# Kernel optimization log

Measured on AMD Instinct MI355X. Metric: run time of the kernel, lower is better.

The kernel has to match this reference:

```python
import jax, jax.numpy as jnp
import numpy as np

D_MODEL = 1024
D = 512
B = 32
L = 1024


def setup_inputs() -> dict:
    key = jax.random.key(0)
    ks = jax.random.split(key, 8)
    s = 1.0 / np.sqrt(D_MODEL)
    x = jax.random.normal(ks[0], (B, L, D_MODEL), dtype=jnp.float32)
    mask = jnp.ones((B, 1, L), dtype=jnp.int32)  # padding mask; 1 = keep
    Wq = jax.random.uniform(ks[1], (D, D_MODEL), jnp.float32, -s, s)
    bq = jax.random.uniform(ks[2], (D,), jnp.float32, -s, s)
    Wk = jax.random.uniform(ks[3], (D, D_MODEL), jnp.float32, -s, s)
    bk = jax.random.uniform(ks[4], (D,), jnp.float32, -s, s)
    Wv = jax.random.uniform(ks[5], (D, D_MODEL), jnp.float32, -s, s)
    bv = jax.random.uniform(ks[6], (D,), jnp.float32, -s, s)
    return {"x": x, "Wq": Wq, "bq": bq, "Wk": Wk, "bk": bk, "Wv": Wv, "bv": bv, "mask": mask}


def reference(x, Wq, bq, Wk, bk, Wv, bv, mask):
    Bq, Lq, _ = x.shape
    q = jnp.einsum('blc,dc->bld', x, Wq) + bq  # [B,L,D]
    k = jnp.einsum('blc,dc->bld', x, Wk) + bk
    v = jnp.einsum('blc,dc->bld', x, Wv) + bv
    scale = k.shape[-1] ** -0.5
    weights = jnp.einsum('bid,bjd->bij', q, k) * scale  # [B,L,L]
    causal = jnp.tril(jnp.ones((Lq, Lq), dtype=bool))
    neg_inf = jnp.float32(-jnp.inf)
    weights = jnp.where(causal[None, :, :], weights, neg_inf)
    weights = jnp.where(mask == 0, neg_inf, weights)  # mask broadcasts [B,1,L]
    weights = jax.nn.softmax(weights, axis=-1)
    # NOTE: source calls self.dropout(weights) but discards result -> no-op
    out = jnp.einsum('bij,bjd->bid', weights, v)
    return jax.nn.relu(out)
```

## Files before the change

### kernel.cpp

```cpp
#include <hip/hip_runtime.h>
#include <hip/hip_bf16.h>
#include <stdint.h>

#define DM 1024
#define DD 512
#define BB 32
#define LL 1024
#define SCALE 0.04419417382415922f
#define MAT ((size_t)BB * LL * DD)

typedef float f32x4 __attribute__((ext_vector_type(4)));
typedef short bf16x8 __attribute__((ext_vector_type(8)));
typedef short bf16x4 __attribute__((ext_vector_type(4)));

__device__ inline unsigned short f2bf(float f) {
    union { float f; uint32_t u; } v; v.f = f;
    uint32_t r = v.u + 0x7fffu + ((v.u >> 16) & 1u);
    return (unsigned short)(r >> 16);
}
__device__ inline float bf2f(unsigned short u) {
    union { uint32_t u; float f; } v; v.u = ((uint32_t)u) << 16;
    return v.f;
}

__device__ inline bf16x4 cvt4(f32x4 a, float s) {
    bf16x4 r;
    r[0] = (short)f2bf(a[0] * s);
    r[1] = (short)f2bf(a[1] * s);
    r[2] = (short)f2bf(a[2] * s);
    r[3] = (short)f2bf(a[3] * s);
    return r;
}

#define GLOAD_LDS16(gsrc, ldst) \
    __builtin_amdgcn_global_load_lds((const __attribute__((address_space(1))) unsigned int*)(gsrc), \
        (__attribute__((address_space(3))) unsigned int*)(ldst), 16, 0, 0)

__device__ inline void publish_barrier() {
    asm volatile("s_waitcnt vmcnt(0)" ::: "memory");
    __builtin_amdgcn_sched_barrier(0);
    __builtin_amdgcn_s_barrier();
    __builtin_amdgcn_sched_barrier(0);
}
__device__ inline void gate6() {
    asm volatile("s_waitcnt vmcnt(6)" ::: "memory");
    __builtin_amdgcn_sched_barrier(0);
    __builtin_amdgcn_s_barrier();
    __builtin_amdgcn_sched_barrier(0);
}
__device__ inline void gate4() {
    asm volatile("s_waitcnt vmcnt(4)" ::: "memory");
    __builtin_amdgcn_sched_barrier(0);
    __builtin_amdgcn_s_barrier();
    __builtin_amdgcn_sched_barrier(0);
}
__device__ inline void gate2() {
    asm volatile("s_waitcnt vmcnt(2)" ::: "memory");
    __builtin_amdgcn_sched_barrier(0);
    __builtin_amdgcn_s_barrier();
    __builtin_amdgcn_sched_barrier(0);
}
__device__ inline void gate0() {
    asm volatile("s_waitcnt vmcnt(0)" ::: "memory");
    __builtin_amdgcn_sched_barrier(0);
    __builtin_amdgcn_s_barrier();
    __builtin_amdgcn_sched_barrier(0);
}
__device__ inline void gateB() {
    __builtin_amdgcn_sched_barrier(0);
    __builtin_amdgcn_s_barrier();
    __builtin_amdgcn_sched_barrier(0);
}

__global__ __launch_bounds__(256) void cast_all(const float* __restrict__ x,
                                                const float* __restrict__ Wq,
                                                const float* __restrict__ Wk,
                                                const float* __restrict__ Wv,
                                                unsigned short* __restrict__ xb,
                                                unsigned short* __restrict__ Wb)
{
    int bx = blockIdx.x;
    if (bx < 16384) {
        size_t idx = (size_t)bx * 256 + threadIdx.x;
        size_t base = idx * 8;
        f32x4 a = *(const f32x4*)(x + base);
        f32x4 b = *(const f32x4*)(x + base + 4);
        bf16x4 lo = cvt4(a, 1.0f), hi = cvt4(b, 1.0f);
        bf16x8 o = {lo[0], lo[1], lo[2], lo[3], hi[0], hi[1], hi[2], hi[3]};
        *(bf16x8*)(xb + base) = o;
    } else {
        size_t idx = (size_t)(bx - 16384) * 256 + threadIdx.x;
        int o = (int)(idx >> 16);
        size_t rem = idx & 65535;
        const float* W = (o == 0) ? Wq : (o == 1) ? Wk : Wv;
        float s = (o == 0) ? SCALE : 1.0f;
        size_t base = rem * 8;
        f32x4 a = *(const f32x4*)(W + base);
        f32x4 b = *(const f32x4*)(W + base + 4);
        bf16x4 lo = cvt4(a, s), hi = cvt4(b, s);
        bf16x8 out = {lo[0], lo[1], lo[2], lo[3], hi[0], hi[1], hi[2], hi[3]};
        *(bf16x8*)(Wb + (size_t)o * 524288 + base) = out;
    }
}

__global__ __launch_bounds__(512, 2) void qkv_proj4(
    const unsigned short* __restrict__ xb,
    const unsigned short* __restrict__ Wb,
    const float* __restrict__ bq, const float* __restrict__ bk, const float* __restrict__ bv,
    unsigned short* __restrict__ qkv)
{
    __shared__ __align__(16) unsigned short AL[2][2][8192];
    __shared__ __align__(16) unsigned short BL[2][2][8192];

    const int o = blockIdx.y;
    const float* bias = (o == 0) ? bq : (o == 1) ? bk : bv;
    const float wscale = (o == 0) ? SCALE : 1.0f;
    const unsigned short* W = Wb + (size_t)o * 524288;
    unsigned short* out = qkv + (size_t)o * MAT;

    int wg = blockIdx.x;
    wg = (wg & 7) * 32 + (wg >> 3);
    const int mt = wg >> 1, nt = wg & 1;
    const int rowbase = mt * 256;
    const int colbase = nt * 256;

    const int tid  = threadIdx.x;
    const int lane = tid & 63;
    const int w    = tid >> 6;
    const int wm   = w >> 2;
    const int wn   = w & 3;
    const int l15  = lane & 15, l4 = lane >> 4;
    const int rxor = l15 & 7;

    const int r8   = lane >> 3;
    const int swch = (lane & 7) ^ r8;

    const char* xpanel = (const char*)(xb + (size_t)rowbase * DM);
    const char* wpanel = (const char*)(W  + (size_t)colbase * DM);

    #define STAGE_HALF(panel, T, H, slot) do {                                   \
        _Pragma("unroll")                                                        \
        for (int i2 = 0; i2 < 2; ++i2) {                                         \
            int grp = i2 * 8 + w;                                                \
            GLOAD_LDS16((panel) + ((size_t)((H) * 128 + grp * 8 + r8) * 2048)    \
                            + (size_t)(T) * 128 + swch * 16,                     \
                        (char*)(slot) + grp * 1024);                             \
        }                                                                        \
    } while (0)

    #define RDA(base, mf4, ks) (*(const bf16x8*)((base) + (wm * 64 + (mf4) * 16 + l15) * 128 \
                            + ((((ks) * 4 + l4) ^ rxor) << 4)))
    #define RDB(base, nfl, ks) (*(const bf16x8*)((base) + (wn * 32 + (nfl) * 16 + l15) * 128 \
                            + ((((ks) * 4 + l4) ^ rxor) << 4)))

    f32x4 acc[8][4];
    #pragma unroll
    for (int i = 0; i < 8; ++i)
        #pragma unroll
        for (int j = 0; j < 4; ++j)
            acc[i][j] = (f32x4){0.f, 0.f, 0.f, 0.f};

    bf16x8 aF[4][2], bF[4][2];

    STAGE_HALF(xpanel, 0, 0, &AL[0][0][0]);
    STAGE_HALF(wpanel, 0, 0, &BL[0][0][0]);
    STAGE_HALF(wpanel, 0, 1, &BL[0][1][0]);
    STAGE_HALF(xpanel, 0, 1, &AL[0][1][0]);

    for (int t = 0; t < 16; ++t) {
        const int c = t & 1, cn = c ^ 1;
        const char* A0b = (const char*)&AL[c][0][0];
        const char* A1b = (const char*)&AL[c][1][0];
        const char* B0b = (const char*)&BL[c][0][0];
        const char* B1b = (const char*)&BL[c][1][0];
        const bool st = (t < 15);

        if (st) { STAGE_HALF(xpanel, t + 1, 0, &AL[cn][0][0]); gate6(); } else gate4();
        #pragma unroll
        for (int ks = 0; ks < 2; ++ks) {
            #pragma unroll
            for (int mf = 0; mf < 4; ++mf) aF[mf][ks] = RDA(A0b, mf, ks);
            bF[0][ks] = RDB(B0b, 0, ks);
            bF[1][ks] = RDB(B0b, 1, ks);
        }
        __builtin_amdgcn_s_setprio(1);
        #pragma unroll
        for (int ks = 0; ks < 2; ++ks)
            #pragma unroll
            for (int nf = 0; nf < 2; ++nf)
                #pragma unroll
                for (int mf = 0; mf < 4; ++mf)
                    acc[mf][nf] = __builtin_amdgcn_mfma_f32_16x16x32_bf16(aF[mf][ks], bF[nf][ks], acc[mf][nf], 0, 0, 0);
        __builtin_amdgcn_s_setprio(0);

        if (st) { STAGE_HALF(wpanel, t + 1, 0, &BL[cn][0][0]); gate6(); } else gate2();
        #pragma unroll
        for (int ks = 0; ks < 2; ++ks) {
            bF[2][ks] = RDB(B1b, 0, ks);
            bF[3][ks] = RDB(B1b, 1, ks);
        }
        __builtin_amdgcn_s_setprio(1);
        #pragma unroll
        for (int ks = 0; ks < 2; ++ks)
            #pragma unroll
            for (int nf = 0; nf < 2; ++nf)
                #pragma unroll
                for (int mf = 0; mf < 4; ++mf)
                    acc[mf][2 + nf] = __builtin_amdgcn_mfma_f32_16x16x32_bf16(aF[mf][ks], bF[2 + nf][ks], acc[mf][2 + nf], 0, 0, 0);
        __builtin_amdgcn_s_setprio(0);

        if (st) { STAGE_HALF(wpanel, t + 1, 1, &BL[cn][1][0]); gate6(); } else gate0();
        #pragma unroll
        for (int ks = 0; ks < 2; ++ks)
            #pragma unroll
            for (int mf = 0; mf < 4; ++mf) aF[mf][ks] = RDA(A1b, mf, ks);
        __builtin_amdgcn_s_setprio(1);
        #pragma unroll
        for (int ks = 0; ks < 2; ++ks)
            #pragma unroll
            for (int nf = 0; nf < 2; ++nf)
                #pragma unroll
                for (int mf = 0; mf < 4; ++mf)
                    acc[4 + mf][nf] = __builtin_amdgcn_mfma_f32_16x16x32_bf16(aF[mf][ks], bF[nf][ks], acc[4 + mf][nf], 0, 0, 0);
        __builtin_amdgcn_s_setprio(0);

        if (st) STAGE_HALF(xpanel, t + 1, 1, &AL[cn][1][0]);
        gateB();
        __builtin_amdgcn_s_setprio(1);
        #pragma unroll
        for (int ks = 0; ks < 2; ++ks)
            #pragma unroll
            for (int nf = 0; nf < 2; ++nf)
                #pragma unroll
                for (int mf = 0; mf < 4; ++mf)
                    acc[4 + mf][2 + nf] = __builtin_amdgcn_mfma_f32_16x16x32_bf16(aF[mf][ks], bF[2 + nf][ks], acc[4 + mf][2 + nf], 0, 0, 0);
        __builtin_amdgcn_s_setprio(0);
    }
    #undef STAGE_HALF
    #undef RDA
    #undef RDB

    #pragma unroll
    for (int nf = 0; nf < 4; ++nf) {
        int col = colbase + ((nf < 2) ? wn * 32 + nf * 16 : 128 + wn * 32 + (nf - 2) * 16) + l15;
        float bv_ = bias[col] * wscale;
        #pragma unroll
        for (int mf = 0; mf < 8; ++mf) {
            int row0 = rowbase + ((mf < 4) ? wm * 64 + mf * 16 : 128 + wm * 64 + (mf - 4) * 16) + l4 * 4;
            #pragma unroll
            for (int r = 0; r < 4; ++r)
                out[(size_t)(row0 + r) * DD + col] = f2bf(acc[mf][nf][r] + bv_);
        }
    }
}

__global__ __launch_bounds__(256) void vtrans(const unsigned short* __restrict__ v,
                                              unsigned short* __restrict__ vt)
{
    __shared__ unsigned short T[64][72];
    const int lt = blockIdx.x, dt = blockIdx.y, b = blockIdx.z;
    const int t = threadIdx.x;
    const unsigned short* src = v + ((size_t)(b * LL + lt * 64)) * DD + dt * 64;
    #pragma unroll
    for (int it = 0; it < 2; ++it) {
        int r  = (t >> 3) + it * 32;
        int c0 = (t & 7) * 8;
        bf16x8 x = *(const bf16x8*)(src + (size_t)r * DD + c0);
        *(bf16x4*)&T[r][c0]     = (bf16x4){x[0], x[1], x[2], x[3]};
        *(bf16x4*)&T[r][c0 + 4] = (bf16x4){x[4], x[5], x[6], x[7]};
    }
    __syncthreads();
    unsigned short* dst = vt + ((size_t)(b * DD + dt * 64)) * LL + lt * 64;
    #pragma unroll
    for (int it = 0; it < 2; ++it) {
        int d  = (t >> 3) + it * 32;
        int c0 = (t & 7) * 8;
        bf16x8 o;
        #pragma unroll
        for (int e = 0; e < 8; ++e) o[e] = T[c0 + e][d];
        *(bf16x8*)(dst + (size_t)d * LL + c0) = o;
    }
}

__global__ __launch_bounds__(256, 2) void sgemm_qk(
    const unsigned short* __restrict__ qkv,
    unsigned short* __restrict__ S)
{
    __shared__ __align__(16) unsigned short At[2][8192];
    __shared__ __align__(16) unsigned short Bt[2][8192];

    int wg = blockIdx.x;
    wg = (wg & 7) * 144 + (wg >> 3);
    const int b = wg / 36;
    const int t36 = wg % 36;
    int mt = 0, accq = 0;
    while (accq + mt + 1 <= t36) { ++mt; accq += mt; }
    const int nt = t36 - accq;

    const int tid  = threadIdx.x;
    const int lane = tid & 63;
    const int w    = tid >> 6;
    const int wr   = (w >> 1) * 64;
    const int wc   = (w & 1) * 64;
    const int l15  = lane & 15, l4 = lane >> 4;

    const int r8   = lane >> 3;
    const int swch = (lane & 7) ^ r8;

    const unsigned short* q = qkv;
    const unsigned short* k = qkv + MAT;
    const char* apanel = (const char*)(q + ((size_t)(b * LL) + mt * 128) * DD);
    const char* bpanel = (const char*)(k + ((size_t)(b * LL) + nt * 128) * DD);

    f32x4 acc[4][4];
    #pragma unroll
    for (int i = 0; i < 4; ++i)
        #pragma unroll
        for (int j = 0; j < 4; ++j)
            acc[i][j] = (f32x4){0.f, 0.f, 0.f, 0.f};

    #define STAGE_QK(KK, BUF) do {                                               \
        _Pragma("unroll")                                                        \
        for (int i2 = 0; i2 < 4; ++i2) {                                         \
            int grp = i2 * 4 + w;                                                \
            size_t rowoff = (size_t)(grp * 8 + r8) * 1024 + (KK) * 2 + swch * 16;\
            GLOAD_LDS16(apanel + rowoff, (char*)&At[BUF][0] + grp * 1024);       \
            GLOAD_LDS16(bpanel + rowoff, (char*)&Bt[BUF][0] + grp * 1024);       \
        }                                                                        \
    } while (0)

    STAGE_QK(0, 0);
    __syncthreads();

    for (int t = 0; t < 8; ++t) {
        const int cur = t & 1;
        if (t < 7) STAGE_QK((t + 1) * 64, cur ^ 1);

        const char* Ab = (const char*)&At[cur][0];
        const char* Bb = (const char*)&Bt[cur][0];
        #pragma unroll
        for (int ks = 0; ks < 2; ++ks) {
            bf16x8 af[4], bf_[4];
            const int ch = (ks * 4 + l4) ^ (l15 & 7);
            #pragma unroll
            for (int m = 0; m < 4; ++m)
                af[m] = *(const bf16x8*)(Ab + (wr + m * 16 + l15) * 128 + (ch << 4));
            #pragma unroll
            for (int n = 0; n < 4; ++n)
                bf_[n] = *(const bf16x8*)(Bb + (wc + n * 16 + l15) * 128 + (ch << 4));
            #pragma unroll
            for (int n = 0; n < 4; ++n)
                #pragma unroll
                for (int m = 0; m < 4; ++m)
                    acc[m][n] = __builtin_amdgcn_mfma_f32_16x16x32_bf16(af[m], bf_[n], acc[m][n], 0, 0, 0);
        }

        if (t < 7) publish_barrier();
    }
    #undef STAGE_QK

    unsigned short* sp = S + ((size_t)(b * LL) + mt * 128) * LL + nt * 128;
    #pragma unroll
    for (int n = 0; n < 4; ++n) {
        int col = wc + n * 16 + l15;
        #pragma unroll
        for (int m = 0; m < 4; ++m) {
            int row0 = wr + m * 16 + l4 * 4;
            #pragma unroll
            for (int r = 0; r < 4; ++r)
                sp[(size_t)(row0 + r) * LL + col] = f2bf(acc[m][n][r]);
        }
    }
}

__global__ __launch_bounds__(256) void softmax_rows(
    const unsigned short* __restrict__ S,
    const int* __restrict__ mask,
    unsigned short* __restrict__ P)
{
    __shared__ float mbias[1024];
    const int rc = blockIdx.x, b = blockIdx.y;
    const int tid = threadIdx.x, lane = tid & 63, w = tid >> 6;

    {
        const int* mp = mask + b * LL;
        #pragma unroll
        for (int j = 0; j < 4; ++j)
            mbias[tid * 4 + j] = mp[tid * 4 + j] ? 0.0f : -1e30f;
    }
    __syncthreads();

    const int j0 = lane * 16;
    for (int i = 0; i < 32; ++i) {
        const int r = rc * 128 + i * 4 + w;
        const unsigned short* srow = S + ((size_t)(b * LL) + r) * LL;

        bf16x8 v0 = {0,0,0,0,0,0,0,0}, v1 = {0,0,0,0,0,0,0,0};
        if (j0 <= r)     v0 = *(const bf16x8*)(srow + j0);
        if (j0 + 8 <= r) v1 = *(const bf16x8*)(srow + j0 + 8);

        float s[16];
        #pragma unroll
        for (int e = 0; e < 8; ++e) {
            int j = j0 + e;
            s[e]     = (j <= r)     ? bf2f((unsigned short)v0[e]) + mbias[j]     : -3e38f;
            s[8 + e] = (j + 8 <= r) ? bf2f((unsigned short)v1[e]) + mbias[j + 8] : -3e38f;
        }
        float mx = s[0];
        #pragma unroll
        for (int e = 1; e < 16; ++e) mx = fmaxf(mx, s[e]);
        mx = fmaxf(mx, __shfl_xor(mx, 1));
        mx = fmaxf(mx, __shfl_xor(mx, 2));
        mx = fmaxf(mx, __shfl_xor(mx, 4));
        mx = fmaxf(mx, __shfl_xor(mx, 8));
        mx = fmaxf(mx, __shfl_xor(mx, 16));
        mx = fmaxf(mx, __shfl_xor(mx, 32));

        float p[16], ls = 0.f;
        #pragma unroll
        for (int e = 0; e < 16; ++e) { p[e] = __expf(s[e] - mx); ls += p[e]; }
        ls += __shfl_xor(ls, 1);
        ls += __shfl_xor(ls, 2);
        ls += __shfl_xor(ls, 4);
        ls += __shfl_xor(ls, 8);
        ls += __shfl_xor(ls, 16);
        ls += __shfl_xor(ls, 32);
        const float inv = 1.0f / ls;

        bf16x8 o0, o1;
        #pragma unroll
        for (int e = 0; e < 8; ++e) {
            o0[e] = (short)f2bf(p[e] * inv);
            o1[e] = (short)f2bf(p[8 + e] * inv);
        }
        unsigned short* prow = P + ((size_t)(b * LL) + r) * LL;
        *(bf16x8*)(prow + j0)     = o0;
        *(bf16x8*)(prow + j0 + 8) = o1;
    }
}

__global__ __launch_bounds__(256, 2) void pv_gemm(
    const unsigned short* __restrict__ P,
    const unsigned short* __restrict__ vt,
    float* __restrict__ outp)
{
    __shared__ __align__(16) unsigned short At[2][8192];
    __shared__ __align__(16) unsigned short Bt[2][8192];

    int wg = blockIdx.x;
    wg = (wg & 7) * 128 + (wg >> 3);
    const int b  = wg >> 5;
    const int rr = wg & 31;
    const int rt = 7 - (rr >> 2);
    const int ct = rr & 3;

    const int tid  = threadIdx.x;
    const int lane = tid & 63;
    const int w    = tid >> 6;
    const int wr   = (w >> 1) * 64;
    const int wc   = (w & 1) * 64;
    const int l15  = lane & 15, l4 = lane >> 4;

    const int r8   = lane >> 3;
    const int swch = (lane & 7) ^ r8;

    const char* apanel = (const char*)(P  + ((size_t)(b * LL) + rt * 128) * LL);
    const char* bpanel = (const char*)(vt + ((size_t)(b * DD) + ct * 128) * LL);

    const int NT = (rt + 1) * 2;

    f32x4 acc[4][4];
    #pragma unroll
    for (int i = 0; i < 4; ++i)
        #pragma unroll
        for (int j = 0; j < 4; ++j)
            acc[i][j] = (f32x4){0.f, 0.f, 0.f, 0.f};

    #define STAGE_PV(KK, BUF) do {                                               \
        _Pragma("unroll")                                                        \
        for (int i2 = 0; i2 < 4; ++i2) {                                         \
            int grp = i2 * 4 + w;                                                \
            size_t rowoff = (size_t)(grp * 8 + r8) * 2048 + (KK) * 2 + swch * 16;\
            GLOAD_LDS16(apanel + rowoff, (char*)&At[BUF][0] + grp * 1024);       \
            GLOAD_LDS16(bpanel + rowoff, (char*)&Bt[BUF][0] + grp * 1024);       \
        }                                                                        \
    } while (0)

    STAGE_PV(0, 0);
    __syncthreads();

    for (int t = 0; t < NT; ++t) {
        const int cur = t & 1;
        if (t < NT - 1) STAGE_PV((t + 1) * 64, cur ^ 1);

        const char* Ab = (const char*)&At[cur][0];
        const char* Bb = (const char*)&Bt[cur][0];
        #pragma unroll
        for (int ks = 0; ks < 2; ++ks) {
            bf16x8 af[4], bf_[4];
            const int ch = (ks * 4 + l4) ^ (l15 & 7);
            #pragma unroll
            for (int m = 0; m < 4; ++m)
                af[m] = *(const bf16x8*)(Ab + (wr + m * 16 + l15) * 128 + (ch << 4));
            #pragma unroll
            for (int n = 0; n < 4; ++n)
                bf_[n] = *(const bf16x8*)(Bb + (wc + n * 16 + l15) * 128 + (ch << 4));
            #pragma unroll
            for (int n = 0; n < 4; ++n)
                #pragma unroll
                for (int m = 0; m < 4; ++m)
                    acc[m][n] = __builtin_amdgcn_mfma_f32_16x16x32_bf16(af[m], bf_[n], acc[m][n], 0, 0, 0);
        }

        if (t < NT - 1) publish_barrier();
    }
    #undef STAGE_PV

    float* op = outp + ((size_t)(b * LL) + rt * 128) * DD + ct * 128;
    #pragma unroll
    for (int n = 0; n < 4; ++n) {
        int col = wc + n * 16 + l15;
        #pragma unroll
        for (int m = 0; m < 4; ++m) {
            int row0 = wr + m * 16 + l4 * 4;
            #pragma unroll
            for (int r = 0; r < 4; ++r)
                op[(size_t)(row0 + r) * DD + col] = fmaxf(acc[m][n][r], 0.f);
        }
    }
}

extern "C" void kernel_launch(void* const* d_in, const int* in_sizes, int n_in,
                              void* d_out, int out_size, void* d_ws, size_t ws_size,
                              hipStream_t stream) {
    const float* x  = (const float*)d_in[0];
    const float* Wq = (const float*)d_in[1];
    const float* bq = (const float*)d_in[2];
    const float* Wk = (const float*)d_in[3];
    const float* bk = (const float*)d_in[4];
    const float* Wv = (const float*)d_in[5];
    const float* bv = (const float*)d_in[6];
    const int* mask = (const int*)d_in[7];

    unsigned short* qkv = (unsigned short*)d_ws;
    unsigned short* v   = qkv + 2 * MAT;
    unsigned short* vtp = qkv + 3 * MAT;
    unsigned short* Wb  = vtp;
    unsigned short* xb  = (unsigned short*)d_out;
    unsigned short* S   = (unsigned short*)d_out;
    unsigned short* Pp  = qkv;
    float* out = (float*)d_out;

    cast_all<<<17152, 256, 0, stream>>>(x, Wq, Wk, Wv, xb, Wb);
    qkv_proj4<<<dim3(256, 3), 512, 0, stream>>>(xb, Wb, bq, bk, bv, qkv);
    vtrans<<<dim3(16, 8, 32), 256, 0, stream>>>(v, vtp);
    sgemm_qk<<<dim3(1152), 256, 0, stream>>>(qkv, S);
    softmax_rows<<<dim3(8, 32), 256, 0, stream>>>(S, mask, Pp);
    pv_gemm<<<dim3(1024), 256, 0, stream>>>(Pp, vtp, out);
}
```

Baseline: 282.0 us.

## Fuse V transpose into QKV projection epilogue and drop setprio hints

```diff
diff --git a/kernel.cpp b/kernel.cpp
--- a/kernel.cpp
+++ b/kernel.cpp
@@ -103,11 +103,12 @@
     }
 }
 
-__global__ __launch_bounds__(512, 2) void qkv_proj4(
+__global__ __launch_bounds__(512, 2) void qkv_proj5(
     const unsigned short* __restrict__ xb,
     const unsigned short* __restrict__ Wb,
     const float* __restrict__ bq, const float* __restrict__ bk, const float* __restrict__ bv,
-    unsigned short* __restrict__ qkv)
+    unsigned short* __restrict__ qkv,
+    unsigned short* __restrict__ vt)
 {
     __shared__ __align__(16) unsigned short AL[2][2][8192];
     __shared__ __align__(16) unsigned short BL[2][2][8192];
@@ -183,7 +184,6 @@
             bF[0][ks] = RDB(B0b, 0, ks);
             bF[1][ks] = RDB(B0b, 1, ks);
         }
-        __builtin_amdgcn_s_setprio(1);
         #pragma unroll
         for (int ks = 0; ks < 2; ++ks)
             #pragma unroll
@@ -191,7 +191,6 @@
                 #pragma unroll
                 for (int mf = 0; mf < 4; ++mf)
                     acc[mf][nf] = __builtin_amdgcn_mfma_f32_16x16x32_bf16(aF[mf][ks], bF[nf][ks], acc[mf][nf], 0, 0, 0);
-        __builtin_amdgcn_s_setprio(0);
 
         if (st) { STAGE_HALF(wpanel, t + 1, 0, &BL[cn][0][0]); gate6(); } else gate2();
         #pragma unroll
@@ -199,7 +198,6 @@
             bF[2][ks] = RDB(B1b, 0, ks);
             bF[3][ks] = RDB(B1b, 1, ks);
         }
-        __builtin_amdgcn_s_setprio(1);
         #pragma unroll
         for (int ks = 0; ks < 2; ++ks)
             #pragma unroll
@@ -207,14 +205,12 @@
                 #pragma unroll
                 for (int mf = 0; mf < 4; ++mf)
                     acc[mf][2 + nf] = __builtin_amdgcn_mfma_f32_16x16x32_bf16(aF[mf][ks], bF[2 + nf][ks], acc[mf][2 + nf], 0, 0, 0);
-        __builtin_amdgcn_s_setprio(0);
 
         if (st) { STAGE_HALF(wpanel, t + 1, 1, &BL[cn][1][0]); gate6(); } else gate0();
         #pragma unroll
         for (int ks = 0; ks < 2; ++ks)
             #pragma unroll
             for (int mf = 0; mf < 4; ++mf) aF[mf][ks] = RDA(A1b, mf, ks);
-        __builtin_amdgcn_s_setprio(1);
         #pragma unroll
         for (int ks = 0; ks < 2; ++ks)
             #pragma unroll
@@ -222,11 +218,9 @@
                 #pragma unroll
                 for (int mf = 0; mf < 4; ++mf)
                     acc[4 + mf][nf] = __builtin_amdgcn_mfma_f32_16x16x32_bf16(aF[mf][ks], bF[nf][ks], acc[4 + mf][nf], 0, 0, 0);
-        __builtin_amdgcn_s_setprio(0);
 
         if (st) STAGE_HALF(xpanel, t + 1, 1, &AL[cn][1][0]);
         gateB();
-        __builtin_amdgcn_s_setprio(1);
         #pragma unroll
         for (int ks = 0; ks < 2; ++ks)
             #pragma unroll
@@ -234,51 +228,63 @@
                 #pragma unroll
                 for (int mf = 0; mf < 4; ++mf)
                     acc[4 + mf][2 + nf] = __builtin_amdgcn_mfma_f32_16x16x32_bf16(aF[mf][ks], bF[2 + nf][ks], acc[4 + mf][2 + nf], 0, 0, 0);
-        __builtin_amdgcn_s_setprio(0);
     }
     #undef STAGE_HALF
     #undef RDA
     #undef RDB
 
-    #pragma unroll
-    for (int nf = 0; nf < 4; ++nf) {
-        int col = colbase + ((nf < 2) ? wn * 32 + nf * 16 : 128 + wn * 32 + (nf - 2) * 16) + l15;
-        float bv_ = bias[col] * wscale;
-        #pragma unroll
-        for (int mf = 0; mf < 8; ++mf) {
-            int row0 = rowbase + ((mf < 4) ? wm * 64 + mf * 16 : 128 + wm * 64 + (mf - 4) * 16) + l4 * 4;
-            #pragma unroll
-            for (int r = 0; r < 4; ++r)
-                out[(size_t)(row0 + r) * DD + col] = f2bf(acc[mf][nf][r] + bv_);
-        }
-    }
-}
-
-__global__ __launch_bounds__(256) void vtrans(const unsigned short* __restrict__ v,
-                                              unsigned short* __restrict__ vt)
-{
-    __shared__ unsigned short T[64][72];
-    const int lt = blockIdx.x, dt = blockIdx.y, b = blockIdx.z;
-    const int t = threadIdx.x;
-    const unsigned short* src = v + ((size_t)(b * LL + lt * 64)) * DD + dt * 64;
-    #pragma unroll
-    for (int it = 0; it < 2; ++it) {
-        int r  = (t >> 3) + it * 32;
-        int c0 = (t & 7) * 8;
-        bf16x8 x = *(const bf16x8*)(src + (size_t)r * DD + c0);
-        *(bf16x4*)&T[r][c0]     = (bf16x4){x[0], x[1], x[2], x[3]};
-        *(bf16x4*)&T[r][c0 + 4] = (bf16x4){x[4], x[5], x[6], x[7]};
-    }
-    __syncthreads();
-    unsigned short* dst = vt + ((size_t)(b * DD + dt * 64)) * LL + lt * 64;
-    #pragma unroll
-    for (int it = 0; it < 2; ++it) {
-        int d  = (t >> 3) + it * 32;
-        int c0 = (t & 7) * 8;
-        bf16x8 o;
-        #pragma unroll
-        for (int e = 0; e < 8; ++e) o[e] = T[c0 + e][d];
-        *(bf16x8*)(dst + (size_t)d * LL + c0) = o;
+    if (o != 2) {
+        #pragma unroll
+        for (int nf = 0; nf < 4; ++nf) {
+            int col = colbase + ((nf < 2) ? wn * 32 + nf * 16 : 128 + wn * 32 + (nf - 2) * 16) + l15;
+            float bv_ = bias[col] * wscale;
+            #pragma unroll
+            for (int mf = 0; mf < 8; ++mf) {
+                int row0 = rowbase + ((mf < 4) ? wm * 64 + mf * 16 : 128 + wm * 64 + (mf - 4) * 16) + l4 * 4;
+                #pragma unroll
+                for (int r = 0; r < 4; ++r)
+                    out[(size_t)(row0 + r) * DD + col] = f2bf(acc[mf][nf][r] + bv_);
+            }
+        }
+    } else {
+        unsigned short* ldsT = (unsigned short*)&AL[0][0][0];
+        const int bidx  = rowbase >> 10;
+        const int lbase = rowbase & 1023;
+        #pragma unroll
+        for (int p = 0; p < 4; ++p) {
+            __syncthreads();
+            #pragma unroll
+            for (int nf = 0; nf < 4; ++nf) {
+                int base16 = (nf < 2) ? wn * 32 + nf * 16 : 128 + wn * 32 + (nf - 2) * 16;
+                if (base16 >= p * 64 && base16 < p * 64 + 64) {
+                    int cc = base16 - p * 64 + l15;
+                    float bv_ = bias[colbase + base16 + l15];
+                    #pragma unroll
+                    for (int mf = 0; mf < 8; ++mf) {
+                        int rowl = ((mf < 4) ? wm * 64 + mf * 16 : 128 + wm * 64 + (mf - 4) * 16) + l4 * 4;
+                        bf16x4 v4;
+                        #pragma unroll
+                        for (int r = 0; r < 4; ++r)
+                            v4[r] = (short)f2bf(acc[mf][nf][r] + bv_);
+                        *(bf16x4*)&ldsT[cc * 264 + rowl] = v4;
+                    }
+                }
+            }
+            __syncthreads();
+            #pragma unroll
+            for (int it = 0; it < 8; ++it) {
+                int u  = tid + it * 512;
+                if (it < 4) {
+                    int uu = tid + it * 512;
+                    int cc = uu >> 5;
+                    int r0 = (uu & 31) * 8;
+                    bf16x8 val = *(const bf16x8*)&ldsT[cc * 264 + r0];
+                    int dg = colbase + p * 64 + cc;
+                    *(bf16x8*)(vt + ((size_t)(bidx * DD + dg)) * LL + lbase + r0) = val;
+                }
+                (void)u;
+            }
+        }
     }
 }
 
@@ -543,17 +549,15 @@
     const int* mask = (const int*)d_in[7];
 
     unsigned short* qkv = (unsigned short*)d_ws;
-    unsigned short* v   = qkv + 2 * MAT;
-    unsigned short* vtp = qkv + 3 * MAT;
-    unsigned short* Wb  = vtp;
+    unsigned short* vtp = qkv + 2 * MAT;
+    unsigned short* Wb  = qkv + 3 * MAT;
     unsigned short* xb  = (unsigned short*)d_out;
     unsigned short* S   = (unsigned short*)d_out;
     unsigned short* Pp  = qkv;
     float* out = (float*)d_out;
 
     cast_all<<<17152, 256, 0, stream>>>(x, Wq, Wk, Wv, xb, Wb);
-    qkv_proj4<<<dim3(256, 3), 512, 0, stream>>>(xb, Wb, bq, bk, bv, qkv);
-    vtrans<<<dim3(16, 8, 32), 256, 0, stream>>>(v, vtp);
+    qkv_proj5<<<dim3(256, 3), 512, 0, stream>>>(xb, Wb, bq, bk, bv, qkv, vtp);
     sgemm_qk<<<dim3(1152), 256, 0, stream>>>(qkv, S);
     softmax_rows<<<dim3(8, 32), 256, 0, stream>>>(S, mask, Pp);
     pv_gemm<<<dim3(1024), 256, 0, stream>>>(Pp, vtp, out);
```

After: 266.0 us. 5.7% less time.
